# Performance work log

Measured on AMD Instinct MI355X. Metric: run time of the kernel, lower is better.

The kernel has to match this reference:

```python
import jax, jax.numpy as jnp
import numpy as np

N_HEAD = 16
HEAD_DIM = 64
EPS_RMS = 1e-6


def _rope(x, cos, sin):
    # x: [B, T, H, D]; cos/sin: [T, D//2] broadcast to [1, T, 1, D//2]
    d2 = x.shape[-1] // 2
    x1, x2 = x[..., :d2], x[..., d2:]
    c = cos[None, :, None, :]
    s = sin[None, :, None, :]
    return jnp.concatenate([x1 * c + x2 * s, -x1 * s + x2 * c], axis=-1)


def _rms_norm(x):
    return x * jax.lax.rsqrt(jnp.mean(x * x, axis=-1, keepdims=True) + EPS_RMS)


def setup_inputs() -> dict:
    key = jax.random.key(0)
    ks = jax.random.split(key, 7)
    B, T, C = 1, 4096, 1024
    x = jax.random.normal(ks[0], (B, T, C), dtype=jnp.float32)
    # realistic rotary angles
    d2 = HEAD_DIM // 2
    inv_freq = 1.0 / (10000.0 ** (np.arange(0, d2, dtype=np.float32) / d2))
    ang = np.arange(T, dtype=np.float32)[:, None] * inv_freq[None, :]
    cos = jnp.asarray(np.cos(ang), dtype=jnp.float32)
    sin = jnp.asarray(np.sin(ang), dtype=jnp.float32)
    scale = 0.02
    wq = jax.random.normal(ks[1], (C, C), dtype=jnp.float32) * scale
    wk = jax.random.normal(ks[2], (C, C), dtype=jnp.float32) * scale
    wv = jax.random.normal(ks[3], (C, C), dtype=jnp.float32) * scale
    wproj = jax.random.normal(ks[4], (C, C), dtype=jnp.float32) * scale
    return {"x": x, "cos": cos, "sin": sin, "wq": wq, "wk": wk, "wv": wv, "wproj": wproj}


def reference(x, cos, sin, wq, wk, wv, wproj):
    B, T, C = x.shape
    H, D = N_HEAD, HEAD_DIM
    # QKV projections (torch Linear: x @ W.T)
    q = (x @ wq.T).reshape(B, T, H, D)
    k = (x @ wk.T).reshape(B, T, H, D)
    v = (x @ wv.T).reshape(B, T, H, D)
    # RoPE then QK RMS-norm
    q = _rms_norm(_rope(q, cos, sin))
    k = _rms_norm(_rope(k, cos, sin))
    # [B, H, T, D]
    q = q.transpose(0, 2, 1, 3)
    k = k.transpose(0, 2, 1, 3)
    v = v.transpose(0, 2, 1, 3)
    scores = jnp.einsum('bhqd,bhkd->bhqk', q, k) * (1.0 / D ** 0.5)
    # causal mask (kv_cache is None, Tq == Tk == T)
    mask = jnp.tril(jnp.ones((T, T), dtype=bool))
    scores = jnp.where(mask[None, None, :, :], scores, -jnp.inf)
    attn = jax.nn.sigmoid(scores)  # sigmoid(-inf) == 0
    y = jnp.einsum('bhqk,bhkd->bhqd', attn, v)
    y = y / (T ** 0.5 + 1e-6)
    y = y.transpose(0, 2, 1, 3).reshape(B, T, C)
    return y @ wproj.T
```

## Files before the change

### kernel.cpp

```cpp
#include <hip/hip_runtime.h>

typedef __attribute__((ext_vector_type(8))) short bf16x8;
typedef __attribute__((ext_vector_type(4))) float f32x4;
typedef __attribute__((ext_vector_type(16))) float f32x16;

__device__ inline f32x4 mfma16(bf16x8 a, bf16x8 b, f32x4 c) {
    return __builtin_amdgcn_mfma_f32_16x16x32_bf16(a, b, c, 0, 0, 0);
}
__device__ inline f32x16 mfma32(bf16x8 a, bf16x8 b, f32x16 c) {
    return __builtin_amdgcn_mfma_f32_32x32x16_bf16(a, b, c, 0, 0, 0);
}

__device__ inline short f2bf(float f) {
    unsigned u = __builtin_bit_cast(unsigned, f);
    unsigned r = (u + 0x7fffu + ((u >> 16) & 1u)) >> 16;
    return (short)r;
}
__device__ inline float bf2f(short h) {
    unsigned u = ((unsigned)(unsigned short)h) << 16;
    return __builtin_bit_cast(float, u);
}

__device__ inline unsigned cvt_pk_bf16(float lo, float hi) {
    unsigned r;
    asm("v_cvt_pk_bf16_f32 %0, %1, %2" : "=v"(r) : "v"(lo), "v"(hi));
    return r;
}
__device__ inline void plane_swap(unsigned& a, unsigned& b) {
    asm("v_permlane32_swap_b32 %0, %1" : "+v"(a), "+v"(b));
}
__device__ inline float exp2_hw(float x) {
    float r;
    asm("v_exp_f32 %0, %1" : "=v"(r) : "v"(x));
    return r;
}

#define GAS(p) (const __attribute__((address_space(1))) void*)(p)
#define LAS(p) (__attribute__((address_space(3))) void*)(p)

#define T_SEQ 4096
#define C_DIM 1024
#define N_HEAD 16
#define HEAD_DIM 64
#define QSCALE (-0.18033688011112042f)
#define INV64 (1.0f / (64.0f + 1e-6f))

__global__ __launch_bounds__(256) void cast5(
    const float* __restrict__ s0, const float* __restrict__ s1,
    const float* __restrict__ s2, const float* __restrict__ s3,
    const float* __restrict__ s4,
    short* __restrict__ d0, short* __restrict__ d1, short* __restrict__ d2,
    short* __restrict__ d3, short* __restrict__ d4,
    int n0, int n1, int n2, int n3, int n4)
{
    int z = blockIdx.y;
    const float* s; short* d; int n;
    switch (z) {
        case 0: s = s0; d = d0; n = n0; break;
        case 1: s = s1; d = d1; n = n1; break;
        case 2: s = s2; d = d2; n = n2; break;
        case 3: s = s3; d = d3; n = n3; break;
        default: s = s4; d = d4; n = n4; break;
    }
    float sc = (z == 4) ? INV64 : 1.0f;
    int i = (blockIdx.x * 256 + threadIdx.x) * 4;
    if (i >= n) return;
    float4 v = *(const float4*)&s[i];
    short4 o;
    o.x = f2bf(v.x * sc); o.y = f2bf(v.y * sc);
    o.z = f2bf(v.z * sc); o.w = f2bf(v.w * sc);
    *(short4*)&d[i] = o;
}

#define QSTAGE(t_, b_) do {                                                      \
    int k0_ = (t_) * 32;                                                         \
    _Pragma("unroll")                                                            \
    for (int s2_ = 0; s2_ < 2; s2_++) {                                          \
        int rbase_ = wave * 32 + s2_ * 16;                                       \
        __builtin_amdgcn_global_load_lds(                                        \
            GAS(&A[(size_t)(row0 + rbase_ + srow) * KK + k0_ + scol]),           \
            LAS(&sA[b_][rbase_ * 32]), 16, 0, 0);                                \
        __builtin_amdgcn_global_load_lds(                                        \
            GAS(&B[(size_t)(col0 + rbase_ + srow) * KK + k0_ + scol]),           \
            LAS(&sB[b_][rbase_ * 32]), 16, 0, 0);                                \
    }                                                                            \
} while (0)

__global__ __launch_bounds__(256) void gemm_qkv(
    const short* __restrict__ A,
    const short* __restrict__ B0, const short* __restrict__ B1,
    const short* __restrict__ B2,
    short* __restrict__ qnb, short* __restrict__ knb, short* __restrict__ vnb,
    const float* __restrict__ cosT, const float* __restrict__ sinT)
{
    int z = blockIdx.z;
    const short* B = (z == 0) ? B0 : ((z == 1) ? B1 : B2);
    short* dst     = (z == 0) ? qnb : ((z == 1) ? knb : vnb);

    __shared__ alignas(16) short sA[2][128 * 32];
    __shared__ alignas(16) short sB[2][128 * 32];

    int tid  = threadIdx.x;
    int wave = tid >> 6, lane = tid & 63;
    int lhi  = lane >> 4, llo = lane & 15;
    int wr   = wave >> 1, wc = wave & 1;
    int row0 = blockIdx.x * 128, col0 = blockIdx.y * 128;
    const int KK = C_DIM;

    int srow = lane >> 2;
    int scol = (lane & 3) * 8;

    f32x4 acc[4][4];
#pragma unroll
    for (int m = 0; m < 4; m++)
#pragma unroll
        for (int n = 0; n < 4; n++)
            acc[m][n] = (f32x4){0.f, 0.f, 0.f, 0.f};

    QSTAGE(0, 0);
    asm volatile("s_waitcnt vmcnt(0)" ::: "memory");
    __builtin_amdgcn_s_barrier();
    int bufg = 0;
    for (int t = 0; t < 32; t++) {
        if (t + 1 < 32) QSTAGE(t + 1, bufg ^ 1);

        bf16x8 af[4], bfv[4];
#pragma unroll
        for (int m = 0; m < 4; m++)
            af[m] = *(const bf16x8*)&sA[bufg][(wr * 64 + m * 16 + llo) * 32 + lhi * 8];
#pragma unroll
        for (int n = 0; n < 4; n++)
            bfv[n] = *(const bf16x8*)&sB[bufg][(wc * 64 + n * 16 + llo) * 32 + lhi * 8];
        __builtin_amdgcn_s_setprio(1);
#pragma unroll
        for (int m = 0; m < 4; m++)
#pragma unroll
            for (int n = 0; n < 4; n++)
                acc[m][n] = mfma16(af[m], bfv[n], acc[m][n]);
        __builtin_amdgcn_s_setprio(0);

        asm volatile("s_waitcnt vmcnt(0)" ::: "memory");
        __builtin_amdgcn_s_barrier();
        bufg ^= 1;
    }

    int hH = blockIdx.y * 2 + wc;
    if (z < 2) {
        float osc = z ? 1.0f : QSCALE;
#pragma unroll
        for (int m = 0; m < 4; m++)
#pragma unroll
            for (int r = 0; r < 4; r++) {
                int row = row0 + wr * 64 + m * 16 + lhi * 4 + r;
                float c0 = cosT[row * 32 + llo],      c1 = cosT[row * 32 + 16 + llo];
                float s0 = sinT[row * 32 + llo],      s1 = sinT[row * 32 + 16 + llo];
                float e0 = acc[m][0][r], e1 = acc[m][1][r];
                float e2 = acc[m][2][r], e3 = acc[m][3][r];
                float r0 = e0 * c0 + e2 * s0;
                float r1 = e1 * c1 + e3 * s1;
                float r2 = e2 * c0 - e0 * s0;
                float r3 = e3 * c1 - e1 * s1;
                float sq = r0 * r0 + r1 * r1 + r2 * r2 + r3 * r3;
                sq += __shfl_xor(sq, 1);
                sq += __shfl_xor(sq, 2);
                sq += __shfl_xor(sq, 4);
                sq += __shfl_xor(sq, 8);
                float inv = rsqrtf(sq * (1.0f / 64.0f) + 1e-6f) * osc;
                size_t base = ((size_t)hH * T_SEQ + row) * HEAD_DIM + llo;
                dst[base +  0] = f2bf(r0 * inv);
                dst[base + 16] = f2bf(r1 * inv);
                dst[base + 32] = f2bf(r2 * inv);
                dst[base + 48] = f2bf(r3 * inv);
            }
    } else {
#pragma unroll
        for (int m = 0; m < 4; m++)
#pragma unroll
            for (int r = 0; r < 4; r++) {
                int row = row0 + wr * 64 + m * 16 + lhi * 4 + r;
                size_t base = ((size_t)hH * T_SEQ + row) * HEAD_DIM + llo;
#pragma unroll
                for (int n = 0; n < 4; n++)
                    dst[base + n * 16] = f2bf(acc[m][n][r]);
            }
    }
}

__global__ __launch_bounds__(256) void gemm_proj(
    const short* __restrict__ A, const short* __restrict__ B,
    float* __restrict__ C, int M, int N, int K)
{
    __shared__ alignas(16) short sA[2][128 * 32];
    __shared__ alignas(16) short sB[2][128 * 32];

    int tid  = threadIdx.x;
    int wave = tid >> 6, lane = tid & 63;
    int lhi  = lane >> 4, llo = lane & 15;
    int wr   = wave >> 1, wc = wave & 1;
    int row0 = blockIdx.x * 128, col0 = blockIdx.y * 128;
    const int KK = K;

    int srow = lane >> 2;
    int scol = (lane & 3) * 8;

    f32x4 acc[4][4];
#pragma unroll
    for (int m = 0; m < 4; m++)
#pragma unroll
        for (int n = 0; n < 4; n++)
            acc[m][n] = (f32x4){0.f, 0.f, 0.f, 0.f};

    int nt = K >> 5;
    QSTAGE(0, 0);
    asm volatile("s_waitcnt vmcnt(0)" ::: "memory");
    __builtin_amdgcn_s_barrier();
    int bufg = 0;
    for (int t = 0; t < nt; t++) {
        if (t + 1 < nt) QSTAGE(t + 1, bufg ^ 1);

        bf16x8 af[4], bfv[4];
#pragma unroll
        for (int m = 0; m < 4; m++)
            af[m] = *(const bf16x8*)&sA[bufg][(wr * 64 + m * 16 + llo) * 32 + lhi * 8];
#pragma unroll
        for (int n = 0; n < 4; n++)
            bfv[n] = *(const bf16x8*)&sB[bufg][(wc * 64 + n * 16 + llo) * 32 + lhi * 8];
        __builtin_amdgcn_s_setprio(1);
#pragma unroll
        for (int m = 0; m < 4; m++)
#pragma unroll
            for (int n = 0; n < 4; n++)
                acc[m][n] = mfma16(af[m], bfv[n], acc[m][n]);
        __builtin_amdgcn_s_setprio(0);

        asm volatile("s_waitcnt vmcnt(0)" ::: "memory");
        __builtin_amdgcn_s_barrier();
        bufg ^= 1;
    }

#pragma unroll
    for (int m = 0; m < 4; m++)
#pragma unroll
        for (int n = 0; n < 4; n++)
#pragma unroll
            for (int r = 0; r < 4; r++) {
                int row = row0 + wr * 64 + m * 16 + lhi * 4 + r;
                int col = col0 + wc * 64 + n * 16 + llo;
                C[(size_t)row * N + col] = acc[m][n][r];
            }
}

__global__ __launch_bounds__(256) void vtrans(
    const short* __restrict__ vnb, short* __restrict__ vt)
{
    __shared__ short sT[64 * 72];
    int h = blockIdx.y, tb = blockIdx.x;
    int tid = threadIdx.x;
#pragma unroll
    for (int p = 0; p < 2; p++) {
        int r  = p * 32 + (tid >> 3);
        int c0 = (tid & 7) * 8;
        bf16x8 v = *(const bf16x8*)&vnb[((size_t)h * T_SEQ + tb * 64 + r) * HEAD_DIM + c0];
#pragma unroll
        for (int j = 0; j < 8; j++) sT[(c0 + j) * 72 + r] = v[j];
    }
    __syncthreads();
#pragma unroll
    for (int p = 0; p < 2; p++) {
        int dd = p * 32 + (tid >> 3);
        int t0 = (tid & 7) * 8;
        bf16x8 o = *(const bf16x8*)&sT[dd * 72 + t0];
        *(bf16x8*)&vt[((size_t)(h * HEAD_DIM + dd)) * T_SEQ + tb * 64 + t0] = o;
    }
}


#define STAGE6(s_, bf_) do {                                                     \
    int kb_ = (s_) * 64;                                                         \
    int r_  = lane >> 3;                                                         \
    int ss_ = (lane & 7) ^ r_;                                                   \
    __builtin_amdgcn_global_load_lds(                                            \
        GAS(Kh + (size_t)(kb_ + wv * 16 + r_) * HEAD_DIM + ss_ * 8),             \
        LAS(Smem + (bf_) * 8192 + (wv * 16) * 128), 16, 0, 0);                   \
    __builtin_amdgcn_global_load_lds(                                            \
        GAS(Kh + (size_t)(kb_ + wv * 16 + 8 + r_) * HEAD_DIM + ss_ * 8),         \
        LAS(Smem + (bf_) * 8192 + (wv * 16 + 8) * 128), 16, 0, 0);               \
    __builtin_amdgcn_global_load_lds(                                            \
        GAS(Vh + (size_t)(wv * 16 + r_) * T_SEQ + kb_ + ss_ * 8),                \
        LAS(Smem + 16384 + (bf_) * 8192 + (wv * 16) * 128), 16, 0, 0);           \
    __builtin_amdgcn_global_load_lds(                                            \
        GAS(Vh + (size_t)(wv * 16 + 8 + r_) * T_SEQ + kb_ + ss_ * 8),            \
        LAS(Smem + 16384 + (bf_) * 8192 + (wv * 16 + 8) * 128), 16, 0, 0);       \
} while (0)

__global__ __launch_bounds__(256, 4) void attn6(
    const short* __restrict__ qn, const short* __restrict__ kn,
    const short* __restrict__ vt, short* __restrict__ yb)
{
    __shared__ alignas(16) char Smem[32768];

    int id = blockIdx.x;
    int h  = id & 15;
    int g  = id >> 4;
    int t  = (g < 16) ? (63 - g) : (g < 32) ? (g - 16)
           : (g < 48) ? (79 - g) : (g - 32);
    int ns = t + 1;

    int tid = threadIdx.x, wv = tid >> 6, lane = tid & 63;
    int lo = lane & 31, hi = lane >> 5;
    int band = wv & 1, tm = wv >> 1;

    const short* Qh = qn + (size_t)h * T_SEQ * HEAD_DIM;
    const short* Kh = kn + (size_t)h * T_SEQ * HEAD_DIM;
    const short* Vh = vt + (size_t)h * HEAD_DIM * T_SEQ;

    int q0 = t * 64;
    int qrow  = q0 + band * 32 + lo;
    int qmaxw = q0 + band * 32 + 31;

    const short* Qr = &Qh[(size_t)qrow * HEAD_DIM + hi * 8];
    bf16x8 qf0 = *(const bf16x8*)&Qr[0];
    bf16x8 qf1 = *(const bf16x8*)&Qr[16];
    bf16x8 qf2 = *(const bf16x8*)&Qr[32];
    bf16x8 qf3 = *(const bf16x8*)&Qr[48];

    f32x16 zed;
#pragma unroll
    for (int r = 0; r < 16; r++) zed[r] = 0.f;

    f32x16 yac0, yac1;
#pragma unroll
    for (int r = 0; r < 16; r++) { yac0[r] = 0.f; yac1[r] = 0.f; }

    unsigned sw   = (unsigned)((lo & 7) << 4);
    unsigned krow = (unsigned)((tm * 32 + lo) * 128);
    unsigned ko0 = krow + ((0u * 32 + hi * 16) ^ sw);
    unsigned ko1 = krow + ((1u * 32 + hi * 16) ^ sw);
    unsigned ko2 = krow + ((2u * 32 + hi * 16) ^ sw);
    unsigned ko3 = krow + ((3u * 32 + hi * 16) ^ sw);
    unsigned vrow0 = (unsigned)(lo * 128)        + 16384u;
    unsigned vrow1 = (unsigned)((32 + lo) * 128) + 16384u;
    unsigned vo00 = vrow0 + (((unsigned)(tm * 64 + 0 * 32 + hi * 16)) ^ sw);
    unsigned vo01 = vrow0 + (((unsigned)(tm * 64 + 1 * 32 + hi * 16)) ^ sw);
    unsigned vo10 = vrow1 + (((unsigned)(tm * 64 + 0 * 32 + hi * 16)) ^ sw);
    unsigned vo11 = vrow1 + (((unsigned)(tm * 64 + 1 * 32 + hi * 16)) ^ sw);

    STAGE6(0, 0);
    int buf = 0;
    for (int s = 0; s < ns; s++) {
        if (s + 1 < ns) {
            STAGE6(s + 1, buf ^ 1);
            asm volatile("s_waitcnt vmcnt(4)" ::: "memory");
        } else {
            asm volatile("s_waitcnt vmcnt(0)" ::: "memory");
        }
        __builtin_amdgcn_s_barrier();

        int kb0 = s * 64 + tm * 32;
        if (kb0 <= qmaxw) {
            const char* B_ = Smem + (buf << 13);
            bf16x8 kf0 = *(const bf16x8*)(B_ + ko0);
            bf16x8 kf1 = *(const bf16x8*)(B_ + ko1);
            bf16x8 kf2 = *(const bf16x8*)(B_ + ko2);
            bf16x8 kf3 = *(const bf16x8*)(B_ + ko3);
            bf16x8 vf00 = *(const bf16x8*)(B_ + vo00);
            bf16x8 vf01 = *(const bf16x8*)(B_ + vo01);
            bf16x8 vf10 = *(const bf16x8*)(B_ + vo10);
            bf16x8 vf11 = *(const bf16x8*)(B_ + vo11);

            f32x16 sv;
            __builtin_amdgcn_s_setprio(1);
            sv = mfma32(kf0, qf0, zed);
            sv = mfma32(kf1, qf1, sv);
            sv = mfma32(kf2, qf2, sv);
            sv = mfma32(kf3, qf3, sv);
            __builtin_amdgcn_s_setprio(0);

            if (kb0 + 31 > q0 + band * 32) {
#pragma unroll
                for (int r = 0; r < 16; r++) {
                    int kvg = kb0 + (r & 3) + 8 * (r >> 2) + 4 * hi;
                    float pv = __builtin_amdgcn_rcpf(1.f + exp2_hw(sv[r]));
                    sv[r] = (kvg <= qrow) ? pv : 0.f;
                }
            } else {
#pragma unroll
                for (int r = 0; r < 16; r++)
                    sv[r] = __builtin_amdgcn_rcpf(1.f + exp2_hw(sv[r]));
            }

#pragma unroll
            for (int k2 = 0; k2 < 2; k2++) {
                unsigned wA = cvt_pk_bf16(sv[8 * k2 + 0], sv[8 * k2 + 1]);
                unsigned wC = cvt_pk_bf16(sv[8 * k2 + 2], sv[8 * k2 + 3]);
                unsigned wB = cvt_pk_bf16(sv[8 * k2 + 4], sv[8 * k2 + 5]);
                unsigned wD = cvt_pk_bf16(sv[8 * k2 + 6], sv[8 * k2 + 7]);
                plane_swap(wA, wB);
                plane_swap(wC, wD);
                union { unsigned u[4]; bf16x8 v; } pw;
                pw.u[0] = wA; pw.u[1] = wC; pw.u[2] = wB; pw.u[3] = wD;
                __builtin_amdgcn_s_setprio(1);
                yac0 = mfma32(pw.v, k2 ? vf01 : vf00, yac0);
                yac1 = mfma32(pw.v, k2 ? vf11 : vf10, yac1);
                __builtin_amdgcn_s_setprio(0);
            }
        }
        asm volatile("" ::: "memory");
        __builtin_amdgcn_s_barrier();
        buf ^= 1;
    }

    __syncthreads();
    float* Yred = (float*)Smem;
    if (tm == 1) {
#pragma unroll
        for (int d = 0; d < 2; d++)
#pragma unroll
            for (int r = 0; r < 16; r++) {
                int crow = (r & 3) + 8 * (r >> 2) + 4 * hi;
                Yred[(band * 32 + crow) * 64 + d * 32 + lo] = d ? yac1[r] : yac0[r];
            }
    }
    __syncthreads();
    if (tm == 0) {
#pragma unroll
        for (int d = 0; d < 2; d++)
#pragma unroll
            for (int r = 0; r < 16; r++) {
                int crow = (r & 3) + 8 * (r >> 2) + 4 * hi;
                float v = (d ? yac1[r] : yac0[r]) + Yred[(band * 32 + crow) * 64 + d * 32 + lo];
                yb[(size_t)(q0 + band * 32 + crow) * C_DIM + h * HEAD_DIM + d * 32 + lo] = f2bf(v);
            }
    }
}

extern "C" void kernel_launch(void* const* d_in, const int* in_sizes, int n_in,
                              void* d_out, int out_size, void* d_ws, size_t ws_size,
                              hipStream_t stream)
{
    const float* x    = (const float*)d_in[0];
    const float* cosT = (const float*)d_in[1];
    const float* sinT = (const float*)d_in[2];
    const float* wq   = (const float*)d_in[3];
    const float* wk   = (const float*)d_in[4];
    const float* wv   = (const float*)d_in[5];
    const float* wp   = (const float*)d_in[6];

    char* ws = (char*)d_ws;
    const size_t MB = 1024 * 1024;
    short* xb    = (short*)(ws + 0);
    short* wqb   = (short*)(ws + 8  * MB);
    short* wkb   = (short*)(ws + 10 * MB);
    short* wvb   = (short*)(ws + 12 * MB);
    short* wpb   = (short*)(ws + 14 * MB);
    short* qnb   = (short*)(ws + 16 * MB);
    short* knb   = (short*)(ws + 24 * MB);
    short* vnb   = (short*)(ws + 32 * MB);
    short* vtb   = (short*)(ws + 40 * MB);
    short* yb    = (short*)(ws + 48 * MB);

    cast5<<<dim3(4096, 5, 1), 256, 0, stream>>>(
        x, wq, wk, wv, wp, xb, wqb, wkb, wvb, wpb,
        T_SEQ * C_DIM, C_DIM * C_DIM, C_DIM * C_DIM, C_DIM * C_DIM, C_DIM * C_DIM);

    gemm_qkv<<<dim3(32, 8, 3), 256, 0, stream>>>(
        xb, wqb, wkb, wvb, qnb, knb, vnb, cosT, sinT);

    vtrans<<<dim3(64, 16, 1), 256, 0, stream>>>(vnb, vtb);

    attn6<<<1024, 256, 0, stream>>>(qnb, knb, vtb, yb);

    gemm_proj<<<dim3(32, 8, 1), 256, 0, stream>>>(
        yb, wpb, (float*)d_out, T_SEQ, C_DIM, C_DIM);
}
```

Baseline: 145.8 us.

## Triple-buffer GEMM LDS staging with partial vmcnt waits and XOR swizzle

Both the QKV and output-projection GEMMs move from double to triple buffering in LDS. Each step prefetches two tiles ahead and waits with a partial vmcnt instead of draining all loads, so global-to-LDS copies can overlap more MFMA work. The LDS column layout is XOR-swizzled on both the write and read side to cut bank conflicts. LDS use grows by half, which could lower occupancy, and a second barrier is added per step.

```diff
diff --git a/kernel.cpp b/kernel.cpp
--- a/kernel.cpp
+++ b/kernel.cpp
@@ -78,12 +78,44 @@
     for (int s2_ = 0; s2_ < 2; s2_++) {                                          \
         int rbase_ = wave * 32 + s2_ * 16;                                       \
         __builtin_amdgcn_global_load_lds(                                        \
-            GAS(&A[(size_t)(row0 + rbase_ + srow) * KK + k0_ + scol]),           \
+            GAS(&A[(size_t)(row0 + rbase_ + srow) * KK + k0_ + scolx]),          \
             LAS(&sA[b_][rbase_ * 32]), 16, 0, 0);                                \
         __builtin_amdgcn_global_load_lds(                                        \
-            GAS(&B[(size_t)(col0 + rbase_ + srow) * KK + k0_ + scol]),           \
+            GAS(&B[(size_t)(col0 + rbase_ + srow) * KK + k0_ + scolx]),          \
             LAS(&sB[b_][rbase_ * 32]), 16, 0, 0);                                \
     }                                                                            \
+} while (0)
+
+#define GEMM_STEP(t_, nt_, bcur_, bnx_) do {                                     \
+    if ((t_) + 2 < (nt_)) {                                                      \
+        QSTAGE((t_) + 2, bnx_);                                                  \
+        asm volatile("s_waitcnt vmcnt(8)" ::: "memory");                         \
+    } else if ((t_) + 1 < (nt_)) {                                               \
+        asm volatile("s_waitcnt vmcnt(4)" ::: "memory");                         \
+    } else {                                                                     \
+        asm volatile("s_waitcnt vmcnt(0)" ::: "memory");                         \
+    }                                                                            \
+    __builtin_amdgcn_s_barrier();                                                \
+    bf16x8 af[4], bfv[4];                                                        \
+    _Pragma("unroll")                                                            \
+    for (int m = 0; m < 4; m++) {                                                \
+        int row_ = wr * 64 + m * 16 + llo;                                       \
+        af[m] = *(const bf16x8*)&sA[bcur_][row_ * 32 + ((lhi ^ (llo & 3)) * 8)]; \
+    }                                                                            \
+    _Pragma("unroll")                                                            \
+    for (int n = 0; n < 4; n++) {                                                \
+        int row_ = wc * 64 + n * 16 + llo;                                       \
+        bfv[n] = *(const bf16x8*)&sB[bcur_][row_ * 32 + ((lhi ^ (llo & 3)) * 8)];\
+    }                                                                            \
+    __builtin_amdgcn_s_setprio(1);                                               \
+    _Pragma("unroll")                                                            \
+    for (int m = 0; m < 4; m++)                                                  \
+        _Pragma("unroll")                                                        \
+        for (int n = 0; n < 4; n++)                                              \
+            acc[m][n] = mfma16(af[m], bfv[n], acc[m][n]);                        \
+    __builtin_amdgcn_s_setprio(0);                                               \
+    asm volatile("" ::: "memory");                                               \
+    __builtin_amdgcn_s_barrier();                                                \
 } while (0)
 
 __global__ __launch_bounds__(256) void gemm_qkv(
@@ -97,8 +129,8 @@
     const short* B = (z == 0) ? B0 : ((z == 1) ? B1 : B2);
     short* dst     = (z == 0) ? qnb : ((z == 1) ? knb : vnb);
 
-    __shared__ alignas(16) short sA[2][128 * 32];
-    __shared__ alignas(16) short sB[2][128 * 32];
+    __shared__ alignas(16) short sA[3][128 * 32];
+    __shared__ alignas(16) short sB[3][128 * 32];
 
     int tid  = threadIdx.x;
     int wave = tid >> 6, lane = tid & 63;
@@ -107,8 +139,8 @@
     int row0 = blockIdx.x * 128, col0 = blockIdx.y * 128;
     const int KK = C_DIM;
 
-    int srow = lane >> 2;
-    int scol = (lane & 3) * 8;
+    int srow  = lane >> 2;
+    int scolx = (((lane & 3) ^ (srow & 3)) * 8);
 
     f32x4 acc[4][4];
 #pragma unroll
@@ -118,30 +150,12 @@
             acc[m][n] = (f32x4){0.f, 0.f, 0.f, 0.f};
 
     QSTAGE(0, 0);
-    asm volatile("s_waitcnt vmcnt(0)" ::: "memory");
-    __builtin_amdgcn_s_barrier();
-    int bufg = 0;
+    QSTAGE(1, 1);
+    int bcur = 0;
     for (int t = 0; t < 32; t++) {
-        if (t + 1 < 32) QSTAGE(t + 1, bufg ^ 1);
-
-        bf16x8 af[4], bfv[4];
-#pragma unroll
-        for (int m = 0; m < 4; m++)
-            af[m] = *(const bf16x8*)&sA[bufg][(wr * 64 + m * 16 + llo) * 32 + lhi * 8];
-#pragma unroll
-        for (int n = 0; n < 4; n++)
-            bfv[n] = *(const bf16x8*)&sB[bufg][(wc * 64 + n * 16 + llo) * 32 + lhi * 8];
-        __builtin_amdgcn_s_setprio(1);
-#pragma unroll
-        for (int m = 0; m < 4; m++)
-#pragma unroll
-            for (int n = 0; n < 4; n++)
-                acc[m][n] = mfma16(af[m], bfv[n], acc[m][n]);
-        __builtin_amdgcn_s_setprio(0);
-
-        asm volatile("s_waitcnt vmcnt(0)" ::: "memory");
-        __builtin_amdgcn_s_barrier();
-        bufg ^= 1;
+        int bnx = bcur + 2; if (bnx >= 3) bnx -= 3;
+        GEMM_STEP(t, 32, bcur, bnx);
+        bcur = bcur + 1; if (bcur >= 3) bcur -= 3;
     }
 
     int hH = blockIdx.y * 2 + wc;
@@ -190,8 +204,8 @@
     const short* __restrict__ A, const short* __restrict__ B,
     float* __restrict__ C, int M, int N, int K)
 {
-    __shared__ alignas(16) short sA[2][128 * 32];
-    __shared__ alignas(16) short sB[2][128 * 32];
+    __shared__ alignas(16) short sA[3][128 * 32];
+    __shared__ alignas(16) short sB[3][128 * 32];
 
     int tid  = threadIdx.x;
     int wave = tid >> 6, lane = tid & 63;
@@ -200,8 +214,8 @@
     int row0 = blockIdx.x * 128, col0 = blockIdx.y * 128;
     const int KK = K;
 
-    int srow = lane >> 2;
-    int scol = (lane & 3) * 8;
+    int srow  = lane >> 2;
+    int scolx = (((lane & 3) ^ (srow & 3)) * 8);
 
     f32x4 acc[4][4];
 #pragma unroll
@@ -212,30 +226,12 @@
 
     int nt = K >> 5;
     QSTAGE(0, 0);
-    asm volatile("s_waitcnt vmcnt(0)" ::: "memory");
-    __builtin_amdgcn_s_barrier();
-    int bufg = 0;
+    QSTAGE(1, 1);
+    int bcur = 0;
     for (int t = 0; t < nt; t++) {
-        if (t + 1 < nt) QSTAGE(t + 1, bufg ^ 1);
-
-        bf16x8 af[4], bfv[4];
-#pragma unroll
-        for (int m = 0; m < 4; m++)
-            af[m] = *(const bf16x8*)&sA[bufg][(wr * 64 + m * 16 + llo) * 32 + lhi * 8];
-#pragma unroll
-        for (int n = 0; n < 4; n++)
-            bfv[n] = *(const bf16x8*)&sB[bufg][(wc * 64 + n * 16 + llo) * 32 + lhi * 8];
-        __builtin_amdgcn_s_setprio(1);
-#pragma unroll
-        for (int m = 0; m < 4; m++)
-#pragma unroll
-            for (int n = 0; n < 4; n++)
-                acc[m][n] = mfma16(af[m], bfv[n], acc[m][n]);
-        __builtin_amdgcn_s_setprio(0);
-
-        asm volatile("s_waitcnt vmcnt(0)" ::: "memory");
-        __builtin_amdgcn_s_barrier();
-        bufg ^= 1;
+        int bnx = bcur + 2; if (bnx >= 3) bnx -= 3;
+        GEMM_STEP(t, nt, bcur, bnx);
+        bcur = bcur + 1; if (bcur >= 3) bcur -= 3;
     }
 
 #pragma unroll
@@ -273,7 +269,6 @@
         *(bf16x8*)&vt[((size_t)(h * HEAD_DIM + dd)) * T_SEQ + tb * 64 + t0] = o;
     }
 }
-
 
 #define STAGE6(s_, bf_) do {                                                     \
     int kb_ = (s_) * 64;                                                         \
```

Result: no change. 145.7 us (-0.0%).
